# Kernel optimization log

Measured on AMD Instinct MI355X. Metric: run time of the kernel, lower is better.

Reference implementation:

```python
import jax, jax.numpy as jnp
import numpy as np

N_NODES = 50000
N_EDGES = 1600000
HIDDEN = 128
HEADS = 8
HEAD_DIM = HIDDEN // HEADS


def setup_inputs() -> dict:
    key = jax.random.key(0)
    ks = jax.random.split(key, 6)
    s = 1.0 / np.sqrt(HIDDEN)
    return {
        "h":   jax.random.normal(ks[0], (N_NODES, HIDDEN), dtype=jnp.float32),
        "W_Q": jax.random.normal(ks[1], (HIDDEN, HIDDEN), dtype=jnp.float32) * s,
        "b_Q": jnp.zeros((HIDDEN,), jnp.float32),
        "W_K": jax.random.normal(ks[2], (HIDDEN, HIDDEN), dtype=jnp.float32) * s,
        "b_K": jnp.zeros((HIDDEN,), jnp.float32),
        "W_V": jax.random.normal(ks[3], (HIDDEN, HIDDEN), dtype=jnp.float32) * s,
        "b_V": jnp.zeros((HIDDEN,), jnp.float32),
        "src": jax.random.randint(ks[4], (N_EDGES,), 0, N_NODES, dtype=jnp.int32),
        "dst": jax.random.randint(ks[5], (N_EDGES,), 0, N_NODES, dtype=jnp.int32),
    }


def _gcn_conv(h, W, b, src, dst, norm_out, norm_in):
    # DGL GraphConv, norm='both', in_feats == out_feats -> aggregate then matmul
    feat = h * norm_out[:, None]                                   # [N, H]
    agg = jax.ops.segment_sum(feat[src], dst, num_segments=N_NODES)  # [N, H]
    agg = agg * norm_in[:, None]
    return agg @ W + b


def reference(h, W_Q, b_Q, W_K, b_K, W_V, b_V, src, dst):
    ones = jnp.ones((N_EDGES,), jnp.float32)
    deg_out = jnp.clip(jax.ops.segment_sum(ones, src, num_segments=N_NODES), 1.0)
    deg_in = jnp.clip(jax.ops.segment_sum(ones, dst, num_segments=N_NODES), 1.0)
    norm_out = jax.lax.rsqrt(deg_out)
    norm_in = jax.lax.rsqrt(deg_in)

    Q = jax.nn.relu(_gcn_conv(h, W_Q, b_Q, src, dst, norm_out, norm_in))
    K = jax.nn.relu(_gcn_conv(h, W_K, b_K, src, dst, norm_out, norm_in))
    V = jax.nn.relu(_gcn_conv(h, W_V, b_V, src, dst, norm_out, norm_in))

    Qh = Q.reshape(N_NODES, HEADS, HEAD_DIM)
    Kh = K.reshape(N_NODES, HEADS, HEAD_DIM)
    Vh = V.reshape(N_NODES, HEADS, HEAD_DIM)

    # per-edge attention: score_e = <K[src], Q[dst]> per head, exp-clamped
    scale = np.sqrt(HEAD_DIM).astype(np.float32)
    score = jnp.sum(Kh[src] * Qh[dst], axis=-1)                    # [E, heads]
    score = jnp.exp(jnp.clip(score / scale, -10.0, 10.0))

    wV = jax.ops.segment_sum(Vh[src] * score[:, :, None], dst, num_segments=N_NODES)  # [N, heads, d]
    z = jax.ops.segment_sum(score, dst, num_segments=N_NODES)     # [N, heads]
    return wV / (z[:, :, None] + 1e-6)
```

## Files before the change

kernel.cpp:

```cpp
#include <hip/hip_runtime.h>

#define N_NODES 50000
#define N_EDGES 1600000
#define CAP 64
#define OVF_CAP 8192

#define O_CNTO   0
#define O_CNTI   50000
#define O_OVFN   100000
#define O_OVF    100002
#define O_BUCKET 120000
#define O_HB     3320000
#define O_AGGB   6520000
#define O_WT     9720000
#define O_Q      9750000
#define O_KV     16150000

typedef unsigned int uint;
typedef __attribute__((ext_vector_type(8))) short short8;
typedef __attribute__((ext_vector_type(4))) float floatx4;

union U16 { uint4 u; short8 s; };

__device__ __forceinline__ uint f2bf2(float a, float b) {
    uint ua = __float_as_uint(a); ua = (ua + 0x7fffu + ((ua >> 16) & 1u)) >> 16;
    uint ub = __float_as_uint(b); ub = (ub + 0x7fffu + ((ub >> 16) & 1u)) >> 16;
    return ua | (ub << 16);
}

__global__ __launch_bounds__(256) void k_build(const int* __restrict__ src,
                                               const int* __restrict__ dst,
                                               int* cnt_out, int* cnt_in,
                                               int* __restrict__ bucket,
                                               int* ovf_n, int2* __restrict__ ovf) {
    int e = blockIdx.x * 256 + threadIdx.x;
    if (e < N_EDGES) {
        int s = src[e], d = dst[e];
        atomicAdd(&cnt_out[s], 1);
        int pos = atomicAdd(&cnt_in[d], 1);
        if (pos < CAP) {
            bucket[(d << 6) + pos] = s;
        } else {
            int o = atomicAdd(ovf_n, 1);
            if (o < OVF_CAP) ovf[o] = make_int2(d, s);
        }
    }
}

__global__ __launch_bounds__(256) void k_wt(const float* __restrict__ WQ,
                                            const float* __restrict__ WK,
                                            const float* __restrict__ WV,
                                            uint* __restrict__ wt) {
    int idx = blockIdx.x * 256 + threadIdx.x;
    if (idx < 3 * 8192) {
        int y = idx >> 13;
        int rem = idx & 8191;
        int k2 = rem >> 7;
        int n  = rem & 127;
        const float* W = (y == 0) ? WQ : (y == 1) ? WK : WV;
        float a = W[(2 * k2) * 128 + n];
        float b = W[(2 * k2 + 1) * 128 + n];
        wt[(y << 13) + (n << 6) + k2] = f2bf2(a, b);
    }
}

__global__ __launch_bounds__(256) void k_hb(const float* __restrict__ h,
                                            const int* __restrict__ cnt_out,
                                            uint* __restrict__ hb) {
    int idx = blockIdx.x * 256 + threadIdx.x;
    if (idx < N_NODES * 64) {
        int n = idx >> 6;
        float no = rsqrtf(fmaxf((float)cnt_out[n], 1.0f));
        float2 hv = *(const float2*)(h + ((size_t)idx << 1));
        hb[idx] = f2bf2(hv.x * no, hv.y * no);
    }
}

__global__ __launch_bounds__(256) void k_agg(
    const int* __restrict__ cnt_in, const int* __restrict__ bucket,
    const int* __restrict__ ovf_n, const int2* __restrict__ ovf,
    const uint* __restrict__ hb, uint* __restrict__ aggb)
{
    int n = blockIdx.x * 4 + (threadIdx.x >> 6);
    int lane = threadIdx.x & 63;
    int cnt = cnt_in[n];
    int m = min(cnt, CAP);
    const int* b = bucket + ((size_t)n << 6);
    float ax = 0.f, ay = 0.f;
    int i = 0;
    for (; i + 4 <= m; i += 4) {
        int s0 = b[i], s1 = b[i + 1], s2 = b[i + 2], s3 = b[i + 3];
        uint u0 = hb[((size_t)s0 << 6) + lane];
        uint u1 = hb[((size_t)s1 << 6) + lane];
        uint u2 = hb[((size_t)s2 << 6) + lane];
        uint u3 = hb[((size_t)s3 << 6) + lane];
        ax += __uint_as_float(u0 << 16) + __uint_as_float(u1 << 16)
            + __uint_as_float(u2 << 16) + __uint_as_float(u3 << 16);
        ay += __uint_as_float(u0 & 0xffff0000u) + __uint_as_float(u1 & 0xffff0000u)
            + __uint_as_float(u2 & 0xffff0000u) + __uint_as_float(u3 & 0xffff0000u);
    }
    for (; i < m; ++i) {
        int s = b[i];
        uint u = hb[((size_t)s << 6) + lane];
        ax += __uint_as_float(u << 16);
        ay += __uint_as_float(u & 0xffff0000u);
    }
    if (cnt > CAP) {
        int on = min(*ovf_n, OVF_CAP);
        for (int j = 0; j < on; ++j) {
            int2 p = ovf[j];
            if (p.x == n) {
                uint u = hb[((size_t)p.y << 6) + lane];
                ax += __uint_as_float(u << 16);
                ay += __uint_as_float(u & 0xffff0000u);
            }
        }
    }
    float ni = rsqrtf(fmaxf((float)cnt, 1.0f));
    aggb[((size_t)n << 6) + lane] = f2bf2(ax * ni, ay * ni);
}

__global__ __launch_bounds__(256) void k_qkv(
    const uint* __restrict__ aggb, const uint* __restrict__ wt,
    const float* __restrict__ bQ, const float* __restrict__ bK,
    const float* __restrict__ bV,
    float* __restrict__ Q, uint* __restrict__ kv)
{
    const int y = blockIdx.y;
    const int row0 = blockIdx.x * 128;
    const float* bias = (y == 0) ? bQ : (y == 1) ? bK : bV;

    __shared__ uint sA[128 * 68];

    const int t = threadIdx.x;
    for (int idx = t; idx < 128 * 16; idx += 256) {
        int r = idx >> 4, c4 = (idx & 15) << 2;
        int row = row0 + r;
        uint4 v = make_uint4(0u, 0u, 0u, 0u);
        if (row < N_NODES) v = *(const uint4*)(aggb + ((size_t)row << 6) + c4);
        *(uint4*)(&sA[r * 68 + c4]) = v;
    }
    __syncthreads();

    const int wave = t >> 6;
    const int lane = t & 63;
    const int mrow = lane & 15;
    const int kq   = lane >> 4;
    const int mbase = wave * 32;
    const uint* wty = wt + (y << 13);

    floatx4 acc[2][8];
    for (int a = 0; a < 2; ++a)
        for (int b = 0; b < 8; ++b)
            acc[a][b] = (floatx4){0.f, 0.f, 0.f, 0.f};

    for (int kc = 0; kc < 128; kc += 32) {
        int koff = (kc >> 1) + (kq << 2);
        short8 afr[2], bfr[8];
        for (int mt = 0; mt < 2; ++mt) {
            U16 u; u.u = *(const uint4*)(&sA[(mbase + mt * 16 + mrow) * 68 + koff]);
            afr[mt] = u.s;
        }
        for (int nt = 0; nt < 8; ++nt) {
            U16 u; u.u = *(const uint4*)(wty + ((nt * 16 + mrow) << 6) + koff);
            bfr[nt] = u.s;
        }
        for (int mt = 0; mt < 2; ++mt)
            for (int nt = 0; nt < 8; ++nt)
                acc[mt][nt] = __builtin_amdgcn_mfma_f32_16x16x32_bf16(
                    afr[mt], bfr[nt], acc[mt][nt], 0, 0, 0);
    }

    if (y == 0) {
        for (int mt = 0; mt < 2; ++mt) {
            int rbase = row0 + mbase + mt * 16 + kq * 4;
            for (int nt = 0; nt < 8; ++nt) {
                int c = nt * 16 + mrow;
                float bv = bias[c];
                for (int r = 0; r < 4; ++r) {
                    int row = rbase + r;
                    if (row < N_NODES)
                        Q[((size_t)row << 7) + c] = fmaxf(acc[mt][nt][r] + bv, 0.f);
                }
            }
        }
    } else {
        const int vo = (y == 2) ? 1 : 0;
        for (int mt = 0; mt < 2; ++mt) {
            int rbase = row0 + mbase + mt * 16 + kq * 4;
            for (int nt = 0; nt < 8; ++nt) {
                int c = nt * 16 + mrow;
                float bv = bias[c];
                for (int r = 0; r < 4; ++r) {
                    float v = fmaxf(acc[mt][nt][r] + bv, 0.f);
                    float pv = __shfl_xor(v, 1);
                    int row = rbase + r;
                    if (((lane & 1) == 0) && row < N_NODES)
                        kv[((size_t)row << 7) + c + vo] = f2bf2(v, pv);
                }
            }
        }
    }
}

__device__ __forceinline__ void attn_step(uint2 kvp, float qx, float qy,
                                          float& ax, float& ay, float& zacc) {
    float p = __uint_as_float(kvp.x << 16) * qx
            + __uint_as_float(kvp.x & 0xffff0000u) * qy;
    p += __shfl_xor(p, 1);
    p += __shfl_xor(p, 2);
    p += __shfl_xor(p, 4);
    float sc = __expf(fminf(fmaxf(p * 0.25f, -10.f), 10.f));
    ax += __uint_as_float(kvp.y << 16) * sc;
    ay += __uint_as_float(kvp.y & 0xffff0000u) * sc;
    zacc += sc;
}

__global__ __launch_bounds__(256) void k_attn(
    const int* __restrict__ cnt_in, const int* __restrict__ bucket,
    const int* __restrict__ ovf_n, const int2* __restrict__ ovf,
    const float* __restrict__ Q, const uint* __restrict__ kv,
    float* __restrict__ out)
{
    int n = blockIdx.x * 4 + (threadIdx.x >> 6);
    int lane = threadIdx.x & 63;
    int cnt = cnt_in[n];
    int m = min(cnt, CAP);
    const int* b = bucket + ((size_t)n << 6);

    float2 q2 = *(const float2*)(Q + ((size_t)n << 7) + (lane << 1));
    float ax = 0.f, ay = 0.f, zacc = 0.f;

    int i = 0;
    for (; i + 4 <= m; i += 4) {
        int s0 = b[i], s1 = b[i + 1], s2 = b[i + 2], s3 = b[i + 3];
        uint2 p0 = *(const uint2*)(kv + ((size_t)s0 << 7) + (lane << 1));
        uint2 p1 = *(const uint2*)(kv + ((size_t)s1 << 7) + (lane << 1));
        uint2 p2 = *(const uint2*)(kv + ((size_t)s2 << 7) + (lane << 1));
        uint2 p3 = *(const uint2*)(kv + ((size_t)s3 << 7) + (lane << 1));
        attn_step(p0, q2.x, q2.y, ax, ay, zacc);
        attn_step(p1, q2.x, q2.y, ax, ay, zacc);
        attn_step(p2, q2.x, q2.y, ax, ay, zacc);
        attn_step(p3, q2.x, q2.y, ax, ay, zacc);
    }
    for (; i < m; ++i) {
        int s = b[i];
        uint2 p = *(const uint2*)(kv + ((size_t)s << 7) + (lane << 1));
        attn_step(p, q2.x, q2.y, ax, ay, zacc);
    }
    if (cnt > CAP) {
        int on = min(*ovf_n, OVF_CAP);
        for (int j = 0; j < on; ++j) {
            int2 pr = ovf[j];
            if (pr.x == n) {
                uint2 p = *(const uint2*)(kv + ((size_t)pr.y << 7) + (lane << 1));
                attn_step(p, q2.x, q2.y, ax, ay, zacc);
            }
        }
    }

    float inv = 1.0f / (zacc + 1e-6f);
    float2 o; o.x = ax * inv; o.y = ay * inv;
    *(float2*)(out + ((size_t)n << 7) + (lane << 1)) = o;
}

extern "C" void kernel_launch(void* const* d_in, const int* in_sizes, int n_in,
                              void* d_out, int out_size, void* d_ws, size_t ws_size,
                              hipStream_t stream) {
    const float* h   = (const float*)d_in[0];
    const float* WQ  = (const float*)d_in[1];
    const float* bQ  = (const float*)d_in[2];
    const float* WK  = (const float*)d_in[3];
    const float* bK  = (const float*)d_in[4];
    const float* WV  = (const float*)d_in[5];
    const float* bV  = (const float*)d_in[6];
    const int*   src = (const int*)d_in[7];
    const int*   dst = (const int*)d_in[8];
    float* out = (float*)d_out;
    float* ws  = (float*)d_ws;
    int*   wsi = (int*)d_ws;

    int*   cnt_out = wsi + O_CNTO;
    int*   cnt_in  = wsi + O_CNTI;
    int*   ovf_n   = wsi + O_OVFN;
    int2*  ovf     = (int2*)(wsi + O_OVF);
    int*   bucket  = wsi + O_BUCKET;
    uint*  hb      = (uint*)(ws + O_HB);
    uint*  aggb    = (uint*)(ws + O_AGGB);
    uint*  wt      = (uint*)(ws + O_WT);
    float* Q       = ws + O_Q;
    uint*  kv      = (uint*)(ws + O_KV);

    hipMemsetAsync(wsi, 0, (2 * N_NODES + 2) * sizeof(int), stream);

    k_wt<<<(3 * 8192 + 255) / 256, 256, 0, stream>>>(WQ, WK, WV, wt);
    k_build<<<N_EDGES / 256, 256, 0, stream>>>(src, dst, cnt_out, cnt_in,
                                               bucket, ovf_n, ovf);
    k_hb<<<(N_NODES * 64 + 255) / 256, 256, 0, stream>>>(h, cnt_out, hb);

    k_agg<<<N_NODES / 4, 256, 0, stream>>>(cnt_in, bucket, ovf_n, ovf, hb, aggb);

    dim3 g_qkv((N_NODES + 127) / 128, 3);
    k_qkv<<<g_qkv, 256, 0, stream>>>(aggb, wt, bQ, bK, bV, Q, kv);

    k_attn<<<N_NODES / 4, 256, 0, stream>>>(cnt_in, bucket, ovf_n, ovf,
                                            Q, kv, out);
}
```

Measured before the change: 474.4 us.

## Split attention lanes across edges per head and store Q as bf16

Q, K and V are now each written as separate bf16 buffers, so Q is stored in bf16 instead of fp32 and K and V are no longer interleaved. The attention kernel switches from one edge per wave-wide iteration to eight edges at once: each lane owns one head and one edge, computes the full 16-element dot product locally, and reduces the V accumulators across the eight edge lanes with shuffles at the end. This removes the per-edge shuffle reduction and serial dependency and reads Q with half the bytes. In exchange each lane holds more registers (16 accumulators plus 16 Q values), makes scattered 32-byte loads, and Q loses precision to bf16.

```diff
diff --git a/kernel.cpp b/kernel.cpp
--- a/kernel.cpp
+++ b/kernel.cpp
@@ -13,8 +13,9 @@
 #define O_HB     3320000
 #define O_AGGB   6520000
 #define O_WT     9720000
-#define O_Q      9750000
-#define O_KV     16150000
+#define O_QB     9750000
+#define O_KB     12950000
+#define O_VB     16150000
 
 typedef unsigned int uint;
 typedef __attribute__((ext_vector_type(8))) short short8;
@@ -27,6 +28,8 @@
     uint ub = __float_as_uint(b); ub = (ub + 0x7fffu + ((ub >> 16) & 1u)) >> 16;
     return ua | (ub << 16);
 }
+__device__ __forceinline__ float bflo(uint u) { return __uint_as_float(u << 16); }
+__device__ __forceinline__ float bfhi(uint u) { return __uint_as_float(u & 0xffff0000u); }
 
 __global__ __launch_bounds__(256) void k_build(const int* __restrict__ src,
                                                const int* __restrict__ dst,
@@ -94,16 +97,14 @@
         uint u1 = hb[((size_t)s1 << 6) + lane];
         uint u2 = hb[((size_t)s2 << 6) + lane];
         uint u3 = hb[((size_t)s3 << 6) + lane];
-        ax += __uint_as_float(u0 << 16) + __uint_as_float(u1 << 16)
-            + __uint_as_float(u2 << 16) + __uint_as_float(u3 << 16);
-        ay += __uint_as_float(u0 & 0xffff0000u) + __uint_as_float(u1 & 0xffff0000u)
-            + __uint_as_float(u2 & 0xffff0000u) + __uint_as_float(u3 & 0xffff0000u);
+        ax += bflo(u0) + bflo(u1) + bflo(u2) + bflo(u3);
+        ay += bfhi(u0) + bfhi(u1) + bfhi(u2) + bfhi(u3);
     }
     for (; i < m; ++i) {
         int s = b[i];
         uint u = hb[((size_t)s << 6) + lane];
-        ax += __uint_as_float(u << 16);
-        ay += __uint_as_float(u & 0xffff0000u);
+        ax += bflo(u);
+        ay += bfhi(u);
     }
     if (cnt > CAP) {
         int on = min(*ovf_n, OVF_CAP);
@@ -111,8 +112,8 @@
             int2 p = ovf[j];
             if (p.x == n) {
                 uint u = hb[((size_t)p.y << 6) + lane];
-                ax += __uint_as_float(u << 16);
-                ay += __uint_as_float(u & 0xffff0000u);
+                ax += bflo(u);
+                ay += bfhi(u);
             }
         }
     }
@@ -124,11 +125,12 @@
     const uint* __restrict__ aggb, const uint* __restrict__ wt,
     const float* __restrict__ bQ, const float* __restrict__ bK,
     const float* __restrict__ bV,
-    float* __restrict__ Q, uint* __restrict__ kv)
+    uint* __restrict__ qb, uint* __restrict__ kb, uint* __restrict__ vb)
 {
     const int y = blockIdx.y;
     const int row0 = blockIdx.x * 128;
     const float* bias = (y == 0) ? bQ : (y == 1) ? bK : bV;
+    uint* obuf = (y == 0) ? qb : (y == 1) ? kb : vb;
 
     __shared__ uint sA[128 * 68];
 
@@ -171,97 +173,116 @@
                     afr[mt], bfr[nt], acc[mt][nt], 0, 0, 0);
     }
 
-    if (y == 0) {
-        for (int mt = 0; mt < 2; ++mt) {
-            int rbase = row0 + mbase + mt * 16 + kq * 4;
-            for (int nt = 0; nt < 8; ++nt) {
-                int c = nt * 16 + mrow;
-                float bv = bias[c];
-                for (int r = 0; r < 4; ++r) {
-                    int row = rbase + r;
-                    if (row < N_NODES)
-                        Q[((size_t)row << 7) + c] = fmaxf(acc[mt][nt][r] + bv, 0.f);
-                }
+    for (int mt = 0; mt < 2; ++mt) {
+        int rbase = row0 + mbase + mt * 16 + kq * 4;
+        for (int nt = 0; nt < 8; ++nt) {
+            int c = nt * 16 + mrow;
+            float bv = bias[c];
+            for (int r = 0; r < 4; ++r) {
+                float v = fmaxf(acc[mt][nt][r] + bv, 0.f);
+                float pv = __shfl_xor(v, 1);
+                int row = rbase + r;
+                if (((lane & 1) == 0) && row < N_NODES)
+                    obuf[((size_t)row << 6) + (c >> 1)] = f2bf2(v, pv);
             }
         }
-    } else {
-        const int vo = (y == 2) ? 1 : 0;
-        for (int mt = 0; mt < 2; ++mt) {
-            int rbase = row0 + mbase + mt * 16 + kq * 4;
-            for (int nt = 0; nt < 8; ++nt) {
-                int c = nt * 16 + mrow;
-                float bv = bias[c];
-                for (int r = 0; r < 4; ++r) {
-                    float v = fmaxf(acc[mt][nt][r] + bv, 0.f);
-                    float pv = __shfl_xor(v, 1);
-                    int row = rbase + r;
-                    if (((lane & 1) == 0) && row < N_NODES)
-                        kv[((size_t)row << 7) + c + vo] = f2bf2(v, pv);
-                }
-            }
-        }
-    }
-}
-
-__device__ __forceinline__ void attn_step(uint2 kvp, float qx, float qy,
-                                          float& ax, float& ay, float& zacc) {
-    float p = __uint_as_float(kvp.x << 16) * qx
-            + __uint_as_float(kvp.x & 0xffff0000u) * qy;
-    p += __shfl_xor(p, 1);
-    p += __shfl_xor(p, 2);
-    p += __shfl_xor(p, 4);
-    float sc = __expf(fminf(fmaxf(p * 0.25f, -10.f), 10.f));
-    ax += __uint_as_float(kvp.y << 16) * sc;
-    ay += __uint_as_float(kvp.y & 0xffff0000u) * sc;
-    zacc += sc;
+    }
 }
 
 __global__ __launch_bounds__(256) void k_attn(
     const int* __restrict__ cnt_in, const int* __restrict__ bucket,
     const int* __restrict__ ovf_n, const int2* __restrict__ ovf,
-    const float* __restrict__ Q, const uint* __restrict__ kv,
-    float* __restrict__ out)
+    const uint* __restrict__ qb, const uint* __restrict__ kb,
+    const uint* __restrict__ vb, float* __restrict__ out)
 {
     int n = blockIdx.x * 4 + (threadIdx.x >> 6);
     int lane = threadIdx.x & 63;
+    int hh = lane >> 3;
+    int g  = lane & 7;
     int cnt = cnt_in[n];
     int m = min(cnt, CAP);
     const int* b = bucket + ((size_t)n << 6);
-
-    float2 q2 = *(const float2*)(Q + ((size_t)n << 7) + (lane << 1));
-    float ax = 0.f, ay = 0.f, zacc = 0.f;
-
-    int i = 0;
-    for (; i + 4 <= m; i += 4) {
-        int s0 = b[i], s1 = b[i + 1], s2 = b[i + 2], s3 = b[i + 3];
-        uint2 p0 = *(const uint2*)(kv + ((size_t)s0 << 7) + (lane << 1));
-        uint2 p1 = *(const uint2*)(kv + ((size_t)s1 << 7) + (lane << 1));
-        uint2 p2 = *(const uint2*)(kv + ((size_t)s2 << 7) + (lane << 1));
-        uint2 p3 = *(const uint2*)(kv + ((size_t)s3 << 7) + (lane << 1));
-        attn_step(p0, q2.x, q2.y, ax, ay, zacc);
-        attn_step(p1, q2.x, q2.y, ax, ay, zacc);
-        attn_step(p2, q2.x, q2.y, ax, ay, zacc);
-        attn_step(p3, q2.x, q2.y, ax, ay, zacc);
-    }
-    for (; i < m; ++i) {
-        int s = b[i];
-        uint2 p = *(const uint2*)(kv + ((size_t)s << 7) + (lane << 1));
-        attn_step(p, q2.x, q2.y, ax, ay, zacc);
-    }
+    int sb = (lane < m) ? b[lane] : 0;
+
+    float qf[16];
+    {
+        const uint* qp = qb + ((size_t)n << 6) + (hh << 3);
+        uint4 a = *(const uint4*)qp;
+        uint4 c = *(const uint4*)(qp + 4);
+        uint uu[8] = {a.x, a.y, a.z, a.w, c.x, c.y, c.z, c.w};
+        #pragma unroll
+        for (int j = 0; j < 8; ++j) { qf[2*j] = bflo(uu[j]); qf[2*j+1] = bfhi(uu[j]); }
+    }
+
+    float vacc[16];
+    #pragma unroll
+    for (int j = 0; j < 16; ++j) vacc[j] = 0.f;
+    float zacc = 0.f;
+
+    for (int i = 0; i < m; i += 8) {
+        int e = i + g;
+        int s = __shfl(sb, e);
+        bool valid = e < m;
+        if (valid) {
+            const uint* kp = kb + ((size_t)s << 6) + (hh << 3);
+            uint4 ka = *(const uint4*)kp;
+            uint4 kc = *(const uint4*)(kp + 4);
+            uint ku[8] = {ka.x, ka.y, ka.z, ka.w, kc.x, kc.y, kc.z, kc.w};
+            float p = 0.f;
+            #pragma unroll
+            for (int j = 0; j < 8; ++j)
+                p += bflo(ku[j]) * qf[2*j] + bfhi(ku[j]) * qf[2*j+1];
+            float sc = __expf(fminf(fmaxf(p * 0.25f, -10.f), 10.f));
+            const uint* vp = vb + ((size_t)s << 6) + (hh << 3);
+            uint4 va = *(const uint4*)vp;
+            uint4 vc = *(const uint4*)(vp + 4);
+            uint vu[8] = {va.x, va.y, va.z, va.w, vc.x, vc.y, vc.z, vc.w};
+            #pragma unroll
+            for (int j = 0; j < 8; ++j) {
+                vacc[2*j]   += sc * bflo(vu[j]);
+                vacc[2*j+1] += sc * bfhi(vu[j]);
+            }
+            zacc += sc;
+        }
+    }
+
     if (cnt > CAP) {
         int on = min(*ovf_n, OVF_CAP);
-        for (int j = 0; j < on; ++j) {
-            int2 pr = ovf[j];
-            if (pr.x == n) {
-                uint2 p = *(const uint2*)(kv + ((size_t)pr.y << 7) + (lane << 1));
-                attn_step(p, q2.x, q2.y, ax, ay, zacc);
+        for (int j2 = 0; j2 < on; ++j2) {
+            int2 pr = ovf[j2];
+            if (pr.x == n && g == 0) {
+                int s = pr.y;
+                const uint* kp = kb + ((size_t)s << 6) + (hh << 3);
+                uint4 ka = *(const uint4*)kp;
+                uint4 kc = *(const uint4*)(kp + 4);
+                uint ku[8] = {ka.x, ka.y, ka.z, ka.w, kc.x, kc.y, kc.z, kc.w};
+                float p = 0.f;
+                for (int j = 0; j < 8; ++j)
+                    p += bflo(ku[j]) * qf[2*j] + bfhi(ku[j]) * qf[2*j+1];
+                float sc = __expf(fminf(fmaxf(p * 0.25f, -10.f), 10.f));
+                const uint* vp = vb + ((size_t)s << 6) + (hh << 3);
+                uint4 va = *(const uint4*)vp;
+                uint4 vc = *(const uint4*)(vp + 4);
+                uint vu[8] = {va.x, va.y, va.z, va.w, vc.x, vc.y, vc.z, vc.w};
+                for (int j = 0; j < 8; ++j) {
+                    vacc[2*j]   += sc * bflo(vu[j]);
+                    vacc[2*j+1] += sc * bfhi(vu[j]);
+                }
+                zacc += sc;
             }
         }
     }
 
+    #pragma unroll
+    for (int mask = 1; mask <= 4; mask <<= 1) {
+        #pragma unroll
+        for (int j = 0; j < 16; ++j) vacc[j] += __shfl_xor(vacc[j], mask);
+        zacc += __shfl_xor(zacc, mask);
+    }
+
     float inv = 1.0f / (zacc + 1e-6f);
-    float2 o; o.x = ax * inv; o.y = ay * inv;
-    *(float2*)(out + ((size_t)n << 7) + (lane << 1)) = o;
+    float2 o; o.x = vacc[2*g] * inv; o.y = vacc[2*g+1] * inv;
+    *(float2*)(out + ((size_t)n << 7) + (hh << 4) + (g << 1)) = o;
 }
 
 extern "C" void kernel_launch(void* const* d_in, const int* in_sizes, int n_in,
@@ -288,8 +309,9 @@
     uint*  hb      = (uint*)(ws + O_HB);
     uint*  aggb    = (uint*)(ws + O_AGGB);
     uint*  wt      = (uint*)(ws + O_WT);
-    float* Q       = ws + O_Q;
-    uint*  kv      = (uint*)(ws + O_KV);
+    uint*  qb      = (uint*)(ws + O_QB);
+    uint*  kb      = (uint*)(ws + O_KB);
+    uint*  vb      = (uint*)(ws + O_VB);
 
     hipMemsetAsync(wsi, 0, (2 * N_NODES + 2) * sizeof(int), stream);
 
@@ -301,8 +323,8 @@
     k_agg<<<N_NODES / 4, 256, 0, stream>>>(cnt_in, bucket, ovf_n, ovf, hb, aggb);
 
     dim3 g_qkv((N_NODES + 127) / 128, 3);
-    k_qkv<<<g_qkv, 256, 0, stream>>>(aggb, wt, bQ, bK, bV, Q, kv);
+    k_qkv<<<g_qkv, 256, 0, stream>>>(aggb, wt, bQ, bK, bV, qb, kb, vb);
 
     k_attn<<<N_NODES / 4, 256, 0, stream>>>(cnt_in, bucket, ovf_n, ovf,
-                                            Q, kv, out);
-}
+                                            qb, kb, vb, out);
+}
```

Measured after the change: 485.1 us. +2.2%, slower.
